# Performance work log

Hardware: AMD Instinct MI355X
Metric: run time of the kernel (lower is better)

The kernel has to match this reference:

```python
import jax, jax.numpy as jnp
import numpy as np

K = 10  # neighbors (k = min(k, N-1); N=4096 >> 10)
EPS = 1e-5  # InstanceNorm eps (torch default)


def knn_idx(coords, k):
    # coords: [B,3,N] -> indices of k nearest neighbors (excluding self) [B,N,k]
    pts = coords.transpose(0, 2, 1)  # [B,N,3]
    sq = jnp.sum(pts * pts, axis=-1)  # [B,N]
    dist = sq[:, :, None] + sq[:, None, :] - 2.0 * jnp.einsum('bnc,bmc->bnm', pts, pts)
    dist = jnp.clip(dist, 1e-12)
    _, idx = jax.lax.top_k(-dist, k + 1)  # ascending distance, sorted
    return idx[:, :, 1:]  # drop self


def graph_feature(idx, feats):
    # feats: [B,C,N], idx: [B,N,k] -> [B,2C,N,k] = [center, neighbor-center]
    neigh = jax.vmap(lambda f, i: f[:, i])(feats, idx)  # [B,C,N,k]
    center = jnp.broadcast_to(feats[..., None], neigh.shape)
    return jnp.concatenate([center, neigh - center], axis=1)


def instance_norm(x):
    # x: [B,C,N,k]; normalize over spatial dims per (batch, channel), no affine
    mu = jnp.mean(x, axis=(2, 3), keepdims=True)
    var = jnp.var(x, axis=(2, 3), keepdims=True)
    return (x - mu) * jax.lax.rsqrt(var + EPS)


def lrelu(x):
    return jnp.where(x >= 0, x, 0.2 * x)


def setup_inputs() -> dict:
    key = jax.random.key(0)
    k1, k2, k3, k4, k5 = jax.random.split(key, 5)
    B, C, N = 4, 128, 4096
    coords = jax.random.normal(k1, (B, 3, N), dtype=jnp.float32)
    features = jax.random.normal(k2, (B, C, N), dtype=jnp.float32)
    W1 = jax.random.normal(k3, (C, 2 * C), dtype=jnp.float32) * 0.05
    W2 = jax.random.normal(k4, (2 * C, 2 * C), dtype=jnp.float32) * 0.05
    W3 = jax.random.normal(k5, (C, 4 * C), dtype=jnp.float32) * 0.05
    return {"coords": coords, "features": features, "W1": W1, "W2": W2, "W3": W3}


def reference(coords, features, W1, W2, W3):
    idx = knn_idx(coords, K)  # same KNN graph used by both EdgeConv stages
    x0 = features  # [B,C,N]
    # stage 1: EdgeConv C -> C
    g1 = graph_feature(idx, x0)  # [B,2C,N,k]
    x1 = lrelu(instance_norm(jnp.einsum('oc,bcnk->bonk', W1, g1)))
    x1 = jnp.max(x1, axis=-1)  # [B,C,N]
    # stage 2: EdgeConv C -> 2C
    g2 = graph_feature(idx, x1)  # [B,2C,N,k] (input C, cat -> 2C)
    x2 = lrelu(instance_norm(jnp.einsum('oc,bcnk->bonk', W2, g2)))
    x2 = jnp.max(x2, axis=-1)  # [B,2C,N]
    # fuse: [x0,x1,x2] -> 4C -> C via conv1x1 + InstanceNorm (spatial = N)
    x3 = jnp.concatenate([x0, x1, x2], axis=1)  # [B,4C,N]
    x3 = jnp.einsum('oc,bcn->bon', W3, x3)[..., None]  # [B,C,N,1]
    x3 = lrelu(instance_norm(x3))[..., 0]  # [B,C,N]
    return x3
```

## Files before the change

kernel.cpp:

```cpp
#include <hip/hip_runtime.h>
#include <math.h>
#include <stdint.h>

#define NB 4
#define NC 128
#define NP 4096
#define KNN 10


__device__ __forceinline__ uint16_t f2bf(float f) {
  uint32_t u = __float_as_uint(f);
  u += 0x7fffu + ((u >> 16) & 1u);
  return (uint16_t)(u >> 16);
}
__device__ __forceinline__ float bf2f(uint16_t h) {
  return __uint_as_float(((uint32_t)h) << 16);
}

__device__ __forceinline__ void async16(const void* g, void* l) {
  __builtin_amdgcn_global_load_lds(
      (const __attribute__((address_space(1))) unsigned int*)g,
      (__attribute__((address_space(3))) unsigned int*)l,
      16, 0, 0);
}

__device__ __forceinline__ uint32_t fsort(float f) {
  uint32_t u = __float_as_uint(f);
  return (u & 0x80000000u) ? ~u : (u | 0x80000000u);
}
__device__ __forceinline__ float funsort(uint32_t k) {
  uint32_t u = (k & 0x80000000u) ? (k & 0x7fffffffu) : ~k;
  return __uint_as_float(u);
}

typedef __bf16 bf16x8 __attribute__((ext_vector_type(8)));
typedef float f32x4 __attribute__((ext_vector_type(4)));

__global__ void k_prep(const float* __restrict__ W1, const float* __restrict__ W2,
                       const float* __restrict__ W3, const float* __restrict__ coords,
                       uint16_t* __restrict__ W1cat, uint16_t* __restrict__ W2cat,
                       uint16_t* __restrict__ W3b,
                       float* __restrict__ stats, float4* __restrict__ pts4) {
  int t = blockIdx.x * 256 + threadIdx.x;
  if (t < 32768) {
    int o = t >> 7, c = t & 127;
    float v;
    if (o < 128) v = W1[o * 256 + c] - W1[o * 256 + 128 + c];
    else         v = W1[(o - 128) * 256 + 128 + c];
    W1cat[t] = f2bf(v);
  } else if (t < 98304) {
    int t2 = t - 32768;
    int o = t2 >> 7, c = t2 & 127;
    float v;
    if (o < 256) v = W2[o * 256 + c] - W2[o * 256 + 128 + c];
    else         v = W2[(o - 256) * 256 + 128 + c];
    W2cat[t2] = f2bf(v);
  } else if (t < 163840) {
    int t2 = t - 98304;
    W3b[t2] = f2bf(W3[t2]);
  } else if (t < 163840 + 8192) {
    stats[t - 163840] = 0.f;
  } else if (t < 163840 + 8192 + 16384) {
    int t2 = t - 163840 - 8192;
    int b = t2 >> 12, n = t2 & 4095;
    const float* cb = coords + b * 12288;
    float x = cb[n], y = cb[4096 + n], z = cb[8192 + n];
    float w = fmaf(x, x, fmaf(y, y, z * z));
    pts4[t2] = make_float4(x, y, z, w);
  }
}

__global__ void k_trans_feat(const float* __restrict__ feat, uint16_t* __restrict__ Xcat) {
  __shared__ float tile[32][33];
  int bid = blockIdx.x;
  int b = bid >> 9;
  int r = bid & 511;
  int n0 = (r >> 2) << 5;
  int c0 = (r & 3) << 5;
  int tx = threadIdx.x & 31, ty = threadIdx.x >> 5;
#pragma unroll
  for (int i = 0; i < 4; i++) {
    int c = c0 + ty + i * 8;
    tile[ty + i * 8][tx] = feat[(b * 128 + c) * 4096 + n0 + tx];
  }
  __syncthreads();
#pragma unroll
  for (int i = 0; i < 4; i++) {
    int n = n0 + ty + i * 8;
    Xcat[((b * 4096 + n) * 512) + c0 + tx] = f2bf(tile[tx][ty + i * 8]);
  }
}

__global__ void k_knn_thr(const float4* __restrict__ pts4, float* __restrict__ candd) {
  int L = blockIdx.x;
  int ch = L & 7;
  int qb = (L >> 3) & 15;
  int b = L >> 7;
  int m0 = ch << 7;
  const float4* pb = pts4 + b * 4096;
  int t = threadIdx.x;
  int q = (qb << 8) + t;
  float4 qp = pb[q];
  float d10[10];
#pragma unroll
  for (int i = 0; i < 10; i++) d10[i] = 1e30f;
#pragma unroll 2
  for (int mm = 0; mm < 128; mm++) {
    int m = m0 + mm;
    float4 p = pb[m];
    float dot = fmaf(qp.x, p.x, fmaf(qp.y, p.y, qp.z * p.z));
    float s = qp.w + p.w;
    float d = fmaf(-2.f, dot, s);
    d = (m == q) ? 1e30f : d;
    if (d < d10[9]) {
      float carry = d;
#pragma unroll
      for (int i = 0; i < 10; i++) {
        float lo = fminf(d10[i], carry);
        carry = fmaxf(d10[i], carry);
        d10[i] = lo;
      }
    }
  }
  int row = b * 4096 + q;
#pragma unroll
  for (int i = 0; i < 10; i++) candd[row * 80 + ch * 10 + i] = d10[i];
}

__global__ void k_knn_merge(const float* __restrict__ candd, float* __restrict__ tq) {
  int gw = blockIdx.x * 4 + (threadIdx.x >> 6);
  int l = threadIdx.x & 63;
  const float* cp = candd + (size_t)gw * 80;
  uint32_t k0 = fsort(cp[l]);
  uint32_t k1 = (l < 16) ? fsort(cp[64 + l]) : 0xFFFFFFFFu;
  uint32_t g = 0;
#pragma unroll
  for (int it = 0; it < 10; it++) {
    uint32_t m = k0 < k1 ? k0 : k1;
#pragma unroll
    for (int s = 1; s < 64; s <<= 1) {
      uint32_t o = __shfl_xor(m, s);
      m = o < m ? o : m;
    }
    g = m;
    if (it < 9) {
      if (k0 == m) k0 = 0xFFFFFFFFu;
      else if (k1 == m) k1 = 0xFFFFFFFFu;
    }
  }
  if (l == 0) tq[gw] = funsort(g);
}

#define CFCAP 112
#define DMARGIN 1e-3f
__global__ __launch_bounds__(256) void k_knn_cf(
    const float4* __restrict__ pts4, const float* __restrict__ tq,
    int* __restrict__ idxout) {
  __shared__ int candi[8 * CFCAP];
  __shared__ int ccnt[8];
  int blk = blockIdx.x;
  int b = blk >> 9;
  int qg = blk & 511;
  int t = threadIdx.x;
  if (t < 8) ccnt[t] = 0;
  const float4* pb = pts4 + b * 4096;
  int qbase = qg * 8;
  float q2x[8], q2y[8], q2z[8], rhs[8];
#pragma unroll
  for (int j = 0; j < 8; j++) {
    float4 qp = pb[qbase + j];
    q2x[j] = -2.f * qp.x; q2y[j] = -2.f * qp.y; q2z[j] = -2.f * qp.z;
    rhs[j] = tq[b * 4096 + qbase + j] + DMARGIN - qp.w;
  }
  __syncthreads();
#pragma unroll 4
  for (int c = 0; c < 16; c++) {
    float4 p = pb[c * 256 + t];
    int m = c * 256 + t;
#pragma unroll
    for (int j = 0; j < 8; j++) {
      float tt = fmaf(q2x[j], p.x, fmaf(q2y[j], p.y, fmaf(q2z[j], p.z, p.w)));
      if (tt <= rhs[j]) {
        int pos = atomicAdd(&ccnt[j], 1);
        if (pos < CFCAP) candi[j * CFCAP + pos] = m;
      }
    }
  }
  __syncthreads();
  int w = t >> 6;
  int l = t & 63;
  for (int k = 0; k < 2; k++) {
    int qloc = w * 2 + k;
    int q2 = qbase + qloc;
    float4 qp2 = pb[q2];
    int c = ccnt[qloc]; c = c < CFCAP ? c : CFCAP;
    unsigned long long k0 = ~0ULL, k1 = ~0ULL;
#pragma unroll
    for (int u = 0; u < 2; u++) {
      int j = u * 64 + l;
      if (j < c) {
        int m = candi[qloc * CFCAP + j];
        float4 p = pb[m];
        float dot = fmaf(qp2.x, p.x, fmaf(qp2.y, p.y, qp2.z * p.z));
        float s = qp2.w + p.w;
        float d = fmaf(-2.f, dot, s);
        d = (m == q2) ? 1e30f : d;
        unsigned long long key = (((unsigned long long)fsort(d)) << 32) | (uint32_t)m;
        if (u == 0) k0 = key; else k1 = key;
      }
    }
    uint32_t keep[10];
#pragma unroll
    for (int it = 0; it < 10; it++) {
      unsigned long long m = k0 < k1 ? k0 : k1;
#pragma unroll
      for (int s = 1; s < 64; s <<= 1) {
        unsigned long long o = __shfl_xor(m, s);
        m = o < m ? o : m;
      }
      keep[it] = (uint32_t)(m & 0xffffffffu);
      if (k0 == m) k0 = ~0ULL;
      else if (k1 == m) k1 = ~0ULL;
    }
    if (l == 0) {
      int orow = b * 4096 + q2;
#pragma unroll
      for (int i = 0; i < 10; i++) idxout[orow * 10 + i] = (int)keep[i];
    }
  }
}

__global__ __launch_bounds__(256) void k_gemm_bf(
    const uint16_t* __restrict__ Xb, int ldx, int xoff,
    const uint16_t* __restrict__ Wb, int ldw,
    float* __restrict__ Y, int ldy, int K,
    uint16_t* __restrict__ Vb, int voff, int vld) {
  __shared__ __align__(16) uint8_t lds[49152];
  const int t = threadIdx.x;
  const int l = t & 63;
  const int wid = t >> 6;
  const int wr = wid & 1, wc = wid >> 1;
  const int p0 = blockIdx.x * 128;
  const int o0 = blockIdx.y * 64;

  const int rA = l >> 3;
  const int cbp = ((l & 7) ^ rA) << 4;
  const int swl = (l & 7) << 4;

  f32x4 acc[4][2];
#pragma unroll
  for (int mi = 0; mi < 4; mi++)
#pragma unroll
    for (int ni = 0; ni < 2; ni++) acc[mi][ni] = (f32x4)0.f;

  auto stage = [&](int k0, int buf) {
    const uint16_t* Xs_ = Xb + (size_t)p0 * ldx + xoff + k0;
    const uint16_t* Ws_ = Wb + (size_t)o0 * ldw + k0;
#pragma unroll
    for (int cc = 0; cc < 4; cc++) {
      int c = wid * 4 + cc;
      const uint8_t* g = (const uint8_t*)(Xs_ + (size_t)(c * 8 + rA) * ldx) + cbp;
      async16(g, &lds[buf * 16384 + c * 1024]);
    }
#pragma unroll
    for (int cc = 0; cc < 2; cc++) {
      int c = wid * 2 + cc;
      const uint8_t* g = (const uint8_t*)(Ws_ + (size_t)(c * 8 + rA) * ldw) + cbp;
      async16(g, &lds[32768 + buf * 8192 + c * 1024]);
    }
  };

  auto compute = [&](int buf) {
    const uint8_t* Ab = &lds[buf * 16384];
    const uint8_t* Bb = &lds[32768 + buf * 8192];
#pragma unroll
    for (int ks = 0; ks < 2; ks++) {
      int cb = ks * 64 + ((l >> 4) << 4);
      bf16x8 bfr[2];
#pragma unroll
      for (int ni = 0; ni < 2; ni++) {
        int n = wc * 32 + ni * 16 + (l & 15);
        bfr[ni] = *(const bf16x8*)(Bb + n * 128 + (cb ^ swl));
      }
#pragma unroll
      for (int mi = 0; mi < 4; mi++) {
        int m = wr * 64 + mi * 16 + (l & 15);
        bf16x8 afr = *(const bf16x8*)(Ab + m * 128 + (cb ^ swl));
        acc[mi][0] = __builtin_amdgcn_mfma_f32_16x16x32_bf16(afr, bfr[0], acc[mi][0], 0, 0, 0);
        acc[mi][1] = __builtin_amdgcn_mfma_f32_16x16x32_bf16(afr, bfr[1], acc[mi][1], 0, 0, 0);
      }
    }
  };

  const int nsteps = K >> 6;
  stage(0, 0);
  for (int s = 0; s < nsteps; s++) {
    __syncthreads();
    if (s + 1 < nsteps) stage((s + 1) << 6, (s + 1) & 1);
    compute(s & 1);
  }

  const bool isv = (Vb != nullptr) && (o0 >= voff);
#pragma unroll
  for (int mi = 0; mi < 4; mi++)
#pragma unroll
    for (int ni = 0; ni < 2; ni++) {
      int col = o0 + wc * 32 + ni * 16 + (l & 15);
      int row0 = p0 + wr * 64 + mi * 16 + (l >> 4) * 4;
#pragma unroll
      for (int j = 0; j < 4; j++) {
        Y[(size_t)(row0 + j) * ldy + col] = acc[mi][ni][j];
        if (isv) Vb[(size_t)(row0 + j) * vld + (col - voff)] = f2bf(acc[mi][ni][j]);
      }
    }
}

template <int O>
__global__ void k_gather(const float* __restrict__ UV, int ld,
                         const uint16_t* __restrict__ Vb,
                         const int* __restrict__ idx,
                         float* __restrict__ M,
                         float* __restrict__ T1, float* __restrict__ T2) {
  int L = blockIdx.x;
  int rx = L & 7;
  int b = rx >> 1;
  int j = ((L >> 3) << 1) + (rx & 1);
  int n0 = j << 4;
  int o = threadIdx.x;
  float a1 = 0.f, a2 = 0.f;
  for (int pi = 0; pi < 16; pi++) {
    int row = b * 4096 + n0 + pi;
    float u = UV[row * ld + o];
    float s1 = 0.f, s2 = 0.f, vmax = -1e30f;
#pragma unroll
    for (int jj = 0; jj < KNN; jj++) {
      int m = idx[row * 10 + jj];
      float v = bf2f(Vb[(size_t)(b * 4096 + m) * O + o]);
      s1 += v;
      float x = u + v;
      s2 = fmaf(x, x, s2);
      vmax = fmaxf(vmax, v);
    }
    M[row * O + o] = vmax;
    a1 += 10.f * u + s1;
    a2 += s2;
  }
  atomicAdd(&T1[b * O + o], a1);
  atomicAdd(&T2[b * O + o], a2);
}

template <int O>
__global__ void k_passB(const float* __restrict__ UV, int ld,
                        const float* __restrict__ M, int coff,
                        const float* __restrict__ T1, const float* __restrict__ T2,
                        uint16_t* __restrict__ Xcat) {
  int t = blockIdx.x * 256 + threadIdx.x;
  int o = t & (O - 1);
  int pn = t / O;
  int b = pn >> 12;
  float mu = T1[b * O + o] * (1.f / 40960.f);
  float e2 = T2[b * O + o] * (1.f / 40960.f);
  float inv = rsqrtf(e2 - mu * mu + 1e-5f);
  float x = (UV[pn * ld + o] + M[pn * O + o] - mu) * inv;
  Xcat[pn * 512 + coff + o] = f2bf(x >= 0.f ? x : 0.2f * x);
}

__global__ void k_stats3(const float* __restrict__ Y3, float* __restrict__ T1, float* __restrict__ T2) {
  int L = blockIdx.x;
  int rx = L & 7;
  int b = rx >> 1;
  int j = ((L >> 3) << 1) + (rx & 1);
  int n0 = j << 4;
  int o = threadIdx.x;
  float a1 = 0.f, a2 = 0.f;
  for (int pi = 0; pi < 16; pi++) {
    float y = Y3[(b * 4096 + n0 + pi) * 128 + o];
    a1 += y;
    a2 = fmaf(y, y, a2);
  }
  atomicAdd(&T1[b * 128 + o], a1);
  atomicAdd(&T2[b * 128 + o], a2);
}

__global__ void k_out(const float* __restrict__ Y3, const float* __restrict__ T1,
                      const float* __restrict__ T2, float* __restrict__ out) {
  __shared__ float tile[32][33];
  int bid = blockIdx.x;
  int b = bid >> 9;
  int r = bid & 511;
  int n0 = (r >> 2) << 5;
  int o0 = (r & 3) << 5;
  int tx = threadIdx.x & 31, ty = threadIdx.x >> 5;
  int o = o0 + tx;
  float mu = T1[b * 128 + o] * (1.f / 4096.f);
  float e2 = T2[b * 128 + o] * (1.f / 4096.f);
  float inv = rsqrtf(e2 - mu * mu + 1e-5f);
#pragma unroll
  for (int i = 0; i < 4; i++) {
    int n = n0 + ty + i * 8;
    float v = (Y3[(b * 4096 + n) * 128 + o] - mu) * inv;
    tile[ty + i * 8][tx] = v >= 0.f ? v : 0.2f * v;
  }
  __syncthreads();
#pragma unroll
  for (int i = 0; i < 4; i++) {
    int oo = o0 + ty + i * 8;
    out[(b * 128 + oo) * 4096 + n0 + tx] = tile[tx][ty + i * 8];
  }
}

extern "C" void kernel_launch(void* const* d_in, const int* in_sizes, int n_in,
                              void* d_out, int out_size, void* d_ws, size_t ws_size,
                              hipStream_t stream) {
  const float* coords   = (const float*)d_in[0];
  const float* features = (const float*)d_in[1];
  const float* W1       = (const float*)d_in[2];
  const float* W2       = (const float*)d_in[3];
  const float* W3       = (const float*)d_in[4];
  float* out = (float*)d_out;

  float*    ws    = (float*)d_ws;
  uint16_t* Xcat  = (uint16_t*)ws;
  float*    UV    = ws + 4194304;
  float*    Mbuf  = ws + 12582912;
  float*    Y3    = Mbuf;
  int*      idxb  = (int*)(ws + 16777216);
  uint16_t* W1cat = (uint16_t*)(ws + 16941056);
  uint16_t* W2cat = (uint16_t*)(ws + 16957440);
  uint16_t* W3b   = (uint16_t*)(ws + 16990208);
  float*    stats = ws + 17022976;
  uint16_t* Vb1   = (uint16_t*)(ws + 17031168);
  uint16_t* Vb2   = (uint16_t*)(ws + 18079744);
  float*  candd = UV;
  float*  tq    = UV + 1310720;
  float4* pts4  = (float4*)(UV + 1327104);

  k_prep<<<736, 256, 0, stream>>>(W1, W2, W3, coords, W1cat, W2cat, W3b, stats, pts4);
  k_trans_feat<<<2048, 256, 0, stream>>>(features, Xcat);
  k_knn_thr<<<512, 256, 0, stream>>>(pts4, candd);
  k_knn_merge<<<4096, 256, 0, stream>>>(candd, tq);
  k_knn_cf<<<2048, 256, 0, stream>>>(pts4, tq, idxb);

  k_gemm_bf<<<dim3(128, 4), 256, 0, stream>>>(Xcat, 512, 0, W1cat, 128, UV, 256, 128,
                                              Vb1, 128, 128);
  k_gather<128><<<1024, 128, 0, stream>>>(UV, 256, Vb1, idxb, Mbuf, stats + 0, stats + 512);
  k_passB<128><<<8192, 256, 0, stream>>>(UV, 256, Mbuf, 128, stats + 0, stats + 512, Xcat);

  k_gemm_bf<<<dim3(128, 8), 256, 0, stream>>>(Xcat, 512, 128, W2cat, 128, UV, 512, 128,
                                              Vb2, 256, 256);
  k_gather<256><<<1024, 256, 0, stream>>>(UV, 512, Vb2, idxb, Mbuf, stats + 1024, stats + 2048);
  k_passB<256><<<16384, 256, 0, stream>>>(UV, 512, Mbuf, 256, stats + 1024, stats + 2048, Xcat);

  k_gemm_bf<<<dim3(128, 2), 256, 0, stream>>>(Xcat, 512, 0, W3b, 512, Y3, 128, 512,
                                              (uint16_t*)nullptr, 0, 0);
  k_stats3<<<1024, 128, 0, stream>>>(Y3, stats + 3072, stats + 3584);
  k_out<<<2048, 256, 0, stream>>>(Y3, stats + 3072, stats + 3584, out);
}
```

Baseline: 176.0 us.

## Fuse final norm stats into GEMM epilogue, store gather max in bf16

The final GEMM now accumulates per-channel sum and sum-of-squares in its epilogue, using wave shuffles and atomics, so the separate stats kernel and its re-read of Y3 go away. The GEMM epilogue also writes the V half only as bf16 instead of writing both fp32 and bf16, cutting store traffic. The neighbor-max buffer M becomes bf16, halving its write and read traffic between the gather and normalize passes, at the cost of some precision in the max term. Y3 is moved to its own workspace region because M no longer covers it.

```diff
diff --git a/kernel.cpp b/kernel.cpp
--- a/kernel.cpp
+++ b/kernel.cpp
@@ -234,7 +234,8 @@
     const uint16_t* __restrict__ Xb, int ldx, int xoff,
     const uint16_t* __restrict__ Wb, int ldw,
     float* __restrict__ Y, int ldy, int K,
-    uint16_t* __restrict__ Vb, int voff, int vld) {
+    uint16_t* __restrict__ Vb, int voff, int vld,
+    float* __restrict__ T1s, float* __restrict__ T2s) {
   __shared__ __align__(16) uint8_t lds[49152];
   const int t = threadIdx.x;
   const int l = t & 63;
@@ -309,17 +310,40 @@
       int row0 = p0 + wr * 64 + mi * 16 + (l >> 4) * 4;
 #pragma unroll
       for (int j = 0; j < 4; j++) {
-        Y[(size_t)(row0 + j) * ldy + col] = acc[mi][ni][j];
         if (isv) Vb[(size_t)(row0 + j) * vld + (col - voff)] = f2bf(acc[mi][ni][j]);
-      }
-    }
+        else     Y[(size_t)(row0 + j) * ldy + col] = acc[mi][ni][j];
+      }
+    }
+
+  if (T1s != nullptr) {
+    int b = p0 >> 12;
+#pragma unroll
+    for (int ni = 0; ni < 2; ni++) {
+      int col = o0 + wc * 32 + ni * 16 + (l & 15);
+      float a1 = 0.f, a2 = 0.f;
+#pragma unroll
+      for (int mi = 0; mi < 4; mi++)
+#pragma unroll
+        for (int j = 0; j < 4; j++) {
+          float y = acc[mi][ni][j];
+          a1 += y;
+          a2 = fmaf(y, y, a2);
+        }
+      a1 += __shfl_xor(a1, 16); a2 += __shfl_xor(a2, 16);
+      a1 += __shfl_xor(a1, 32); a2 += __shfl_xor(a2, 32);
+      if ((l >> 4) == 0) {
+        atomicAdd(&T1s[b * 128 + col], a1);
+        atomicAdd(&T2s[b * 128 + col], a2);
+      }
+    }
+  }
 }
 
 template <int O>
 __global__ void k_gather(const float* __restrict__ UV, int ld,
                          const uint16_t* __restrict__ Vb,
                          const int* __restrict__ idx,
-                         float* __restrict__ M,
+                         uint16_t* __restrict__ M,
                          float* __restrict__ T1, float* __restrict__ T2) {
   int L = blockIdx.x;
   int rx = L & 7;
@@ -341,7 +365,7 @@
       s2 = fmaf(x, x, s2);
       vmax = fmaxf(vmax, v);
     }
-    M[row * O + o] = vmax;
+    M[(size_t)row * O + o] = f2bf(vmax);
     a1 += 10.f * u + s1;
     a2 += s2;
   }
@@ -351,7 +375,7 @@
 
 template <int O>
 __global__ void k_passB(const float* __restrict__ UV, int ld,
-                        const float* __restrict__ M, int coff,
+                        const uint16_t* __restrict__ M, int coff,
                         const float* __restrict__ T1, const float* __restrict__ T2,
                         uint16_t* __restrict__ Xcat) {
   int t = blockIdx.x * 256 + threadIdx.x;
@@ -361,25 +385,8 @@
   float mu = T1[b * O + o] * (1.f / 40960.f);
   float e2 = T2[b * O + o] * (1.f / 40960.f);
   float inv = rsqrtf(e2 - mu * mu + 1e-5f);
-  float x = (UV[pn * ld + o] + M[pn * O + o] - mu) * inv;
+  float x = (UV[pn * ld + o] + bf2f(M[(size_t)pn * O + o]) - mu) * inv;
   Xcat[pn * 512 + coff + o] = f2bf(x >= 0.f ? x : 0.2f * x);
-}
-
-__global__ void k_stats3(const float* __restrict__ Y3, float* __restrict__ T1, float* __restrict__ T2) {
-  int L = blockIdx.x;
-  int rx = L & 7;
-  int b = rx >> 1;
-  int j = ((L >> 3) << 1) + (rx & 1);
-  int n0 = j << 4;
-  int o = threadIdx.x;
-  float a1 = 0.f, a2 = 0.f;
-  for (int pi = 0; pi < 16; pi++) {
-    float y = Y3[(b * 4096 + n0 + pi) * 128 + o];
-    a1 += y;
-    a2 = fmaf(y, y, a2);
-  }
-  atomicAdd(&T1[b * 128 + o], a1);
-  atomicAdd(&T2[b * 128 + o], a2);
 }
 
 __global__ void k_out(const float* __restrict__ Y3, const float* __restrict__ T1,
@@ -422,8 +429,8 @@
   float*    ws    = (float*)d_ws;
   uint16_t* Xcat  = (uint16_t*)ws;
   float*    UV    = ws + 4194304;
-  float*    Mbuf  = ws + 12582912;
-  float*    Y3    = Mbuf;
+  uint16_t* Mbuf  = (uint16_t*)(ws + 12582912);
+  float*    Y3    = ws + 14680064;
   int*      idxb  = (int*)(ws + 16777216);
   uint16_t* W1cat = (uint16_t*)(ws + 16941056);
   uint16_t* W2cat = (uint16_t*)(ws + 16957440);
@@ -442,17 +449,17 @@
   k_knn_cf<<<2048, 256, 0, stream>>>(pts4, tq, idxb);
 
   k_gemm_bf<<<dim3(128, 4), 256, 0, stream>>>(Xcat, 512, 0, W1cat, 128, UV, 256, 128,
-                                              Vb1, 128, 128);
+                                              Vb1, 128, 128, nullptr, nullptr);
   k_gather<128><<<1024, 128, 0, stream>>>(UV, 256, Vb1, idxb, Mbuf, stats + 0, stats + 512);
   k_passB<128><<<8192, 256, 0, stream>>>(UV, 256, Mbuf, 128, stats + 0, stats + 512, Xcat);
 
   k_gemm_bf<<<dim3(128, 8), 256, 0, stream>>>(Xcat, 512, 128, W2cat, 128, UV, 512, 128,
-                                              Vb2, 256, 256);
+                                              Vb2, 256, 256, nullptr, nullptr);
   k_gather<256><<<1024, 256, 0, stream>>>(UV, 512, Vb2, idxb, Mbuf, stats + 1024, stats + 2048);
   k_passB<256><<<16384, 256, 0, stream>>>(UV, 512, Mbuf, 256, stats + 1024, stats + 2048, Xcat);
 
   k_gemm_bf<<<dim3(128, 2), 256, 0, stream>>>(Xcat, 512, 0, W3b, 512, Y3, 128, 512,
-                                              (uint16_t*)nullptr, 0, 0);
-  k_stats3<<<1024, 128, 0, stream>>>(Y3, stats + 3072, stats + 3584);
+                                              (uint16_t*)nullptr, 0, 0,
+                                              stats + 3072, stats + 3584);
   k_out<<<2048, 256, 0, stream>>>(Y3, stats + 3072, stats + 3584, out);
 }
```

Result: faster. 166.2 us (-5.6%).
